# Kernel tuning notes

Hardware: AMD Instinct MI355X
Metric: run time of the kernel (lower is better)

The kernel has to match this reference:

```python
import jax, jax.numpy as jnp
import numpy as np

B, K, DIM = 4096, 64, 512


def setup_inputs() -> dict:
    key = jax.random.key(0)
    k1, k2, k3 = jax.random.split(key, 3)
    inputs = jax.random.normal(k1, (B, DIM), dtype=jnp.float32)
    decoded = jax.random.normal(k2, (B, K, DIM), dtype=jnp.float32)
    labels = jax.random.randint(k3, (B,), 0, K, dtype=jnp.int64)
    return {"inputs": inputs, "decoded": decoded, "labels": labels, "obj": 0}


def reference(inputs, decoded, labels, obj):
    b = labels.shape[0]
    if obj:
        # gather the label-indexed reconstruction per row, global L2 distance / B
        decoded_tar = decoded[jnp.arange(b), labels]  # (B, dim)
        return jnp.sqrt(jnp.sum(jnp.square(inputs - decoded_tar))) / b
    # obj=False: exclude the label row per batch element, then sum(exp(-||.||^2)).
    # Instead of materializing a boolean mask + masked_select (as in torch),
    # compute the score for all K and zero out the label entry — same math.
    diff = inputs[:, None, :] - decoded               # (B, K, dim)
    mse_all = -jnp.sum(jnp.square(diff), axis=-1)     # (B, K)
    keep = jnp.arange(decoded.shape[1])[None, :] != labels[:, None]  # (B, K)
    return jnp.sum(jnp.where(keep, jnp.exp(mse_all), 0.0))
```

## Files before the change

kernel.cpp:

```cpp
#include <hip/hip_runtime.h>


#define B_SZ 4096
#define K_SZ 64
#define DIM  512
#define ROW_F4 (DIM / 4)
#define SKIP_T 128.0f

template <typename LT>
__global__ __launch_bounds__(256) void score_kernel(
    const float* __restrict__ inputs,
    const float* __restrict__ decoded,
    const LT*    __restrict__ labels,
    float* __restrict__ partials)
{
    const int b    = blockIdx.x;
    const int tid  = threadIdx.x;
    const int wave = tid >> 6;
    const int lane = tid & 63;
    const int m    = lane & 31;
    const int g    = lane >> 5;

    const float4* inp = (const float4*)(inputs + (size_t)b * DIM);
    const float4 in1 = inp[m];

    const int lab = (int)labels[b];
    const float4* dec = (const float4*)(decoded + (size_t)b * K_SZ * DIM);

    const int kbase = wave * 16 + g;

    float s[8];
    #pragma unroll
    for (int j = 0; j < 8; ++j) {
        const float4 d = dec[(size_t)(kbase + 2 * j) * ROW_F4 + m];
        float dx, t;
        dx = in1.x - d.x; t  = dx * dx;
        dx = in1.y - d.y; t += dx * dx;
        dx = in1.z - d.z; t += dx * dx;
        dx = in1.w - d.w; t += dx * dx;
        s[j] = t;
    }

    #pragma unroll
    for (int j = 0; j < 8; ++j) {
        float t = s[j];
        #pragma unroll
        for (int off = 16; off; off >>= 1)
            t += __shfl_xor(t, off, 64);
        s[j] = t;
    }

    float acc = 0.0f;
    #pragma unroll
    for (int j = 0; j < 8; ++j) {
        const int k = kbase + 2 * j;
        float sv = s[j];
        if (__any(sv < SKIP_T)) {
            const float4* rowt = dec + (size_t)k * ROW_F4;
            float t = 0.0f;
            #pragma unroll
            for (int c = 1; c < 4; ++c) {
                const float4 dv = rowt[c * 32 + m];
                const float4 iv = inp[c * 32 + m];
                float dx;
                dx = iv.x - dv.x; t += dx * dx;
                dx = iv.y - dv.y; t += dx * dx;
                dx = iv.z - dv.z; t += dx * dx;
                dx = iv.w - dv.w; t += dx * dx;
            }
            #pragma unroll
            for (int off = 16; off; off >>= 1)
                t += __shfl_xor(t, off, 64);
            sv += t;
        }
        if (sv < SKIP_T && k != lab) acc += expf(-sv);
    }

    acc += __shfl_xor(acc, 32, 64);

    __shared__ float wacc[4];
    if (lane == 0) wacc[wave] = acc;
    __syncthreads();
    if (tid == 0) partials[b] = wacc[0] + wacc[1] + wacc[2] + wacc[3];
}

__global__ __launch_bounds__(256) void reduce_kernel(
    const float* __restrict__ partials, float* __restrict__ out)
{
    float s = 0.0f;
    for (int i = threadIdx.x; i < B_SZ; i += 256) s += partials[i];
    #pragma unroll
    for (int off = 32; off; off >>= 1)
        s += __shfl_xor(s, off, 64);
    __shared__ float wacc[4];
    const int wave = threadIdx.x >> 6, lane = threadIdx.x & 63;
    if (lane == 0) wacc[wave] = s;
    __syncthreads();
    if (threadIdx.x == 0) out[0] = wacc[0] + wacc[1] + wacc[2] + wacc[3];
}

extern "C" void kernel_launch(void* const* d_in, const int* in_sizes, int n_in,
                              void* d_out, int out_size, void* d_ws, size_t ws_size,
                              hipStream_t stream) {
    const float* inputs  = (const float*)d_in[0];
    const float* decoded = (const float*)d_in[1];
    float* out      = (float*)d_out;
    float* partials = (float*)d_ws;

    if (in_sizes[2] >= (int)(B_SZ * sizeof(long long))) {
        score_kernel<long long><<<B_SZ, 256, 0, stream>>>(
            inputs, decoded, (const long long*)d_in[2], partials);
    } else {
        score_kernel<int><<<B_SZ, 256, 0, stream>>>(
            inputs, decoded, (const int*)d_in[2], partials);
    }
    reduce_kernel<<<1, 256, 0, stream>>>(partials, out);
}
```

Measured before the change: 599.2 us.

## Prune distances in two stages using 64-dim partial sums per 16-lane group

Each wave now splits into four 16-lane groups, each handling one decoded row. A first pass over only 64 dimensions gives a lower bound on the squared distance. Rows whose partial sum stays under the threshold then read the next 64 dims, and only if still under the threshold is the full 512-dim distance recomputed. The threshold drops to 104, where exp(-sv) is negligible in fp32. The aim is to cut the bytes read per row for pruned rows, at the cost of extra divergent branches, shuffles and re-reading data in the rare full path. The final reduction also loads partials as float4.

```diff
diff --git a/kernel.cpp b/kernel.cpp
--- a/kernel.cpp
+++ b/kernel.cpp
@@ -5,7 +5,7 @@
 #define K_SZ 64
 #define DIM  512
 #define ROW_F4 (DIM / 4)
-#define SKIP_T 128.0f
+#define SKIP_T 104.0f
 
 template <typename LT>
 __global__ __launch_bounds__(256) void score_kernel(
@@ -18,21 +18,22 @@
     const int tid  = threadIdx.x;
     const int wave = tid >> 6;
     const int lane = tid & 63;
-    const int m    = lane & 31;
-    const int g    = lane >> 5;
+    const int q    = (lane >> 4) & 3;
+    const int m16  = lane & 15;
 
     const float4* inp = (const float4*)(inputs + (size_t)b * DIM);
-    const float4 in1 = inp[m];
+    const float4 in1 = inp[m16];
+    const float4 in2 = inp[16 + m16];
 
     const int lab = (int)labels[b];
     const float4* dec = (const float4*)(decoded + (size_t)b * K_SZ * DIM);
 
-    const int kbase = wave * 16 + g;
+    const int kbase = wave * 16 + q;
 
-    float s[8];
+    float s[4];
     #pragma unroll
-    for (int j = 0; j < 8; ++j) {
-        const float4 d = dec[(size_t)(kbase + 2 * j) * ROW_F4 + m];
+    for (int j = 0; j < 4; ++j) {
+        const float4 d = dec[(size_t)(kbase + 4 * j) * ROW_F4 + m16];
         float dx, t;
         dx = in1.x - d.x; t  = dx * dx;
         dx = in1.y - d.y; t += dx * dx;
@@ -42,40 +43,60 @@
     }
 
     #pragma unroll
-    for (int j = 0; j < 8; ++j) {
+    for (int j = 0; j < 4; ++j) {
         float t = s[j];
         #pragma unroll
-        for (int off = 16; off; off >>= 1)
+        for (int off = 8; off; off >>= 1)
             t += __shfl_xor(t, off, 64);
         s[j] = t;
     }
 
     float acc = 0.0f;
     #pragma unroll
-    for (int j = 0; j < 8; ++j) {
-        const int k = kbase + 2 * j;
+    for (int j = 0; j < 4; ++j) {
+        const int k = kbase + 4 * j;
+        const float4* row = dec + (size_t)k * ROW_F4;
         float sv = s[j];
+
         if (__any(sv < SKIP_T)) {
-            const float4* rowt = dec + (size_t)k * ROW_F4;
-            float t = 0.0f;
-            #pragma unroll
-            for (int c = 1; c < 4; ++c) {
-                const float4 dv = rowt[c * 32 + m];
-                const float4 iv = inp[c * 32 + m];
+            float t2 = 0.0f;
+            if (sv < SKIP_T) {
+                const float4 d2 = row[16 + m16];
                 float dx;
-                dx = iv.x - dv.x; t += dx * dx;
-                dx = iv.y - dv.y; t += dx * dx;
-                dx = iv.z - dv.z; t += dx * dx;
-                dx = iv.w - dv.w; t += dx * dx;
+                dx = in2.x - d2.x; t2  = dx * dx;
+                dx = in2.y - d2.y; t2 += dx * dx;
+                dx = in2.z - d2.z; t2 += dx * dx;
+                dx = in2.w - d2.w; t2 += dx * dx;
             }
             #pragma unroll
-            for (int off = 16; off; off >>= 1)
-                t += __shfl_xor(t, off, 64);
-            sv += t;
+            for (int off = 8; off; off >>= 1)
+                t2 += __shfl_xor(t2, off, 64);
+            sv += t2;
+
+            if (__any(sv < SKIP_T)) {
+                float t3 = 0.0f;
+                if (sv < SKIP_T) {
+                    #pragma unroll
+                    for (int c = 0; c < 8; ++c) {
+                        const float4 dv = row[c * 16 + m16];
+                        const float4 iv = inp[c * 16 + m16];
+                        float dx;
+                        dx = iv.x - dv.x; t3 += dx * dx;
+                        dx = iv.y - dv.y; t3 += dx * dx;
+                        dx = iv.z - dv.z; t3 += dx * dx;
+                        dx = iv.w - dv.w; t3 += dx * dx;
+                    }
+                }
+                #pragma unroll
+                for (int off = 8; off; off >>= 1)
+                    t3 += __shfl_xor(t3, off, 64);
+                if (sv < SKIP_T) sv = t3;
+            }
         }
         if (sv < SKIP_T && k != lab) acc += expf(-sv);
     }
 
+    acc += __shfl_xor(acc, 16, 64);
     acc += __shfl_xor(acc, 32, 64);
 
     __shared__ float wacc[4];
@@ -87,8 +108,12 @@
 __global__ __launch_bounds__(256) void reduce_kernel(
     const float* __restrict__ partials, float* __restrict__ out)
 {
+    const float4* p4 = (const float4*)partials;
     float s = 0.0f;
-    for (int i = threadIdx.x; i < B_SZ; i += 256) s += partials[i];
+    for (int i = threadIdx.x; i < B_SZ / 4; i += 256) {
+        const float4 v = p4[i];
+        s += (v.x + v.y) + (v.z + v.w);
+    }
     #pragma unroll
     for (int off = 32; off; off >>= 1)
         s += __shfl_xor(s, off, 64);
```

Result: no change. 588.9 us (-1.7%).
